# Kernel tuning notes

Hardware: AMD Instinct MI355X
Metric: run time of the kernel (lower is better)

## Reference

```python
import jax, jax.numpy as jnp
import numpy as np
from jax import lax

B, T, H, DEPTH = 32, 2048, 256, 4  # batch, max seq len, hidden, num dilated layers


def setup_inputs() -> dict:
    key = jax.random.key(0)
    k0, k1, k2, k3, k4 = jax.random.split(key, 5)
    x = jax.random.normal(k0, (B, T, H), dtype=jnp.float32)
    # ragged lengths in [T//2, T]
    seq_lens = jax.random.randint(k1, (B,), T // 2, T + 1)
    s = 1.0 / np.sqrt(H)
    Wx = jax.random.uniform(k2, (DEPTH, H, H), jnp.float32, -s, s)
    Wh = jax.random.uniform(k3, (DEPTH, H, H), jnp.float32, -s, s)
    b = jax.random.uniform(k4, (DEPTH, H), jnp.float32, -s, s)
    return {"x": x, "Wx": Wx, "Wh": Wh, "b": b, "seq_lens": seq_lens}


def _dilated_layer(x, Wx, Wh, b, dilation):
    # x: [B, T, H]; recurrence h_k = tanh(x_k @ Wx + h_{k-dilation} @ Wh + b),
    # h_prev = 0 for k < dilation. Positions k mod dilation == r form an
    # independent stream, so reshape into `dilation` interleaved streams and
    # run one scan of length ceil(T/dilation).
    Bn, Tn, Hn = x.shape
    pad = (-Tn) % dilation
    xp = jnp.pad(x, ((0, 0), (0, pad), (0, 0)))
    steps = xp.shape[1] // dilation
    # [steps, B, dilation, H]; element [t, b, r] is timestep t*dilation + r
    xs = jnp.transpose(xp.reshape(Bn, steps, dilation, Hn), (1, 0, 2, 3))
    h0 = jnp.zeros((Bn, dilation, Hn), x.dtype)  # init_state per stream

    def step(h, xt):
        h_new = jnp.tanh(xt @ Wx + h @ Wh + b)
        return h_new, h_new

    _, ys = lax.scan(step, h0, xs)  # [steps, B, dilation, H]
    ys = jnp.transpose(ys, (1, 0, 2, 3)).reshape(Bn, steps * dilation, Hn)
    return ys[:, :Tn]


def reference(x, Wx, Wh, b, seq_lens):
    # Mirrors DilatedRNN.forward: output[i][j][k] for depth j with link_len 2**j.
    # Invalid positions (k >= seq_len) never feed into valid ones (forward-only
    # dilated dependence), so we compute densely and mask at the end.
    depth = Wx.shape[0]
    h = x
    outs = []
    for j in range(depth):
        h = _dilated_layer(h, Wx[j], Wh[j], b[j], 2 ** j)
        outs.append(h)
    out = jnp.stack(outs, axis=1)  # [B, depth, T, H] == output TensorArray
    mask = (jnp.arange(out.shape[2])[None, :] < seq_lens[:, None]).astype(x.dtype)
    return out * mask[:, None, :, None]
```

## Files before the change

kernel.cpp:

```cpp
#include <hip/hip_runtime.h>

#define Bn 32
#define Tn 2048
#define Hn 256
#define DEPTHn 4

typedef _Float16 h2 __attribute__((ext_vector_type(2)));
typedef _Float16 h8 __attribute__((ext_vector_type(8)));

__device__ __forceinline__ h2 pkrtz(float a, float b) {
    return __builtin_bit_cast(h2, __builtin_amdgcn_cvt_pkrtz(a, b));
}

template <int CTRL>
__device__ __forceinline__ float dpp_qp(float x) {
    int xi = __builtin_bit_cast(int, x);
    int r = __builtin_amdgcn_update_dpp(0, xi, CTRL, 0xF, 0xF, true);
    return __builtin_bit_cast(float, r);
}

#define GR 64
__global__ __launch_bounds__(256, 2) void gemm_xw(
    const float* __restrict__ in, long in_bstride,
    const float* __restrict__ Wx, const float* __restrict__ bias,
    float* __restrict__ Z)
{
    __shared__ __align__(16) float a_lds[GR][264];

    const int tid = threadIdx.x;
    const int row0 = blockIdx.x * GR;

    #pragma unroll
    for (int q = 0; q < 16; ++q) {
        int f = tid + q * 256;
        int r  = f >> 6;
        int c4 = f & 63;
        int grow = row0 + r;
        int b = grow >> 11;
        int t = grow & (Tn - 1);
        float4 v = *(const float4*)(in + (long)b * in_bstride + (long)t * Hn + c4 * 4);
        *(float4*)(&a_lds[r][c4 * 4]) = v;
    }
    __syncthreads();

    const int g  = tid >> 5;
    const int cg = tid & 31;

    float acc[8][8];
    #pragma unroll
    for (int i = 0; i < 8; ++i)
        #pragma unroll
        for (int j = 0; j < 8; ++j) acc[i][j] = 0.f;

    for (int k4 = 0; k4 < 64; ++k4) {
        float4 w[4][2];
        #pragma unroll
        for (int kk = 0; kk < 4; ++kk) {
            const float* wr = Wx + (long)(k4 * 4 + kk) * Hn + cg * 8;
            w[kk][0] = *(const float4*)(wr);
            w[kk][1] = *(const float4*)(wr + 4);
        }
        float4 a[8];
        #pragma unroll
        for (int i = 0; i < 8; ++i)
            a[i] = *(const float4*)(&a_lds[i * 8 + g][k4 * 4]);

        #pragma unroll
        for (int i = 0; i < 8; ++i) {
            #pragma unroll
            for (int kk = 0; kk < 4; ++kk) {
                float av = ((const float*)&a[i])[kk];
                acc[i][0] = fmaf(av, w[kk][0].x, acc[i][0]);
                acc[i][1] = fmaf(av, w[kk][0].y, acc[i][1]);
                acc[i][2] = fmaf(av, w[kk][0].z, acc[i][2]);
                acc[i][3] = fmaf(av, w[kk][0].w, acc[i][3]);
                acc[i][4] = fmaf(av, w[kk][1].x, acc[i][4]);
                acc[i][5] = fmaf(av, w[kk][1].y, acc[i][5]);
                acc[i][6] = fmaf(av, w[kk][1].z, acc[i][6]);
                acc[i][7] = fmaf(av, w[kk][1].w, acc[i][7]);
            }
        }
    }

    float4 b0 = *(const float4*)(bias + cg * 8);
    float4 b1 = *(const float4*)(bias + cg * 8 + 4);
    #pragma unroll
    for (int i = 0; i < 8; ++i) {
        long row = row0 + i * 8 + g;
        float4 o0 = { acc[i][0] + b0.x, acc[i][1] + b0.y, acc[i][2] + b0.z, acc[i][3] + b0.w };
        float4 o1 = { acc[i][4] + b1.x, acc[i][5] + b1.y, acc[i][6] + b1.z, acc[i][7] + b1.w };
        *(float4*)(Z + row * Hn + cg * 8)     = o0;
        *(float4*)(Z + row * Hn + cg * 8 + 4) = o1;
    }
}

__global__ __launch_bounds__(512) void rnn_layer(
    const float* __restrict__ Z,
    const float* __restrict__ Wh,
    float* __restrict__ out,
    const int* __restrict__ seq_lens,
    int dilation)
{
    __shared__ __align__(16) h2 hbuf[2 * 144];

    const int tid  = threadIdx.x;
    const int wv   = tid >> 6;
    const int lane = tid & 63;
    const int q    = lane & 3;
    const int c    = lane >> 2;
    const int ch0  = wv * 32 + c;
    const int ch1  = ch0 + 16;

    const int s = blockIdx.x;
    const int b = s / dilation;
    const int r = s % dilation;

    h2 wA[32], wB[32];
    #pragma unroll
    for (int p = 0; p < 32; ++p) {
        int k0 = 64 * q + 2 * p;
        wA[p] = pkrtz(Wh[(long)k0 * Hn + ch0], Wh[(long)(k0 + 1) * Hn + ch0]);
        wB[p] = pkrtz(Wh[(long)k0 * Hn + ch1], Wh[(long)(k0 + 1) * Hn + ch1]);
    }

    if (tid < 288) ((unsigned int*)hbuf)[tid] = 0u;
    const int L = seq_lens[b];
    __syncthreads();

    const float* zb = Z + (long)b * Tn * Hn;
    float* ob = out + (long)b * (DEPTHn * Tn * Hn);

    const int och = (q & 1) ? ch1 : ch0;
    const bool producer = (q < 2);

    int cur = 0;
    float z1 = 0.f, z2 = 0.f;
    if (producer) {
        z1 = zb[(long)r * Hn + och];
        if (r + dilation < Tn) z2 = zb[(long)(r + dilation) * Hn + och];
    }

    for (int t = r; t < Tn; t += dilation) {
        float zc = z1;
        z1 = z2;
        int t2 = t + 2 * dilation;
        if (producer && t2 < Tn) z2 = zb[(long)t2 * Hn + och];

        const h2* hp = &hbuf[cur * 144 + q * 36];
        float a0 = 0.f, a1 = 0.f, a2 = 0.f, a3 = 0.f;
        float b0 = 0.f, b1 = 0.f, b2 = 0.f, b3 = 0.f;
        #pragma unroll
        for (int i4 = 0; i4 < 8; ++i4) {
            h8 hv = *(const h8*)(hp + i4 * 4);
            h2 p0 = __builtin_shufflevector(hv, hv, 0, 1);
            h2 p1 = __builtin_shufflevector(hv, hv, 2, 3);
            h2 p2 = __builtin_shufflevector(hv, hv, 4, 5);
            h2 p3 = __builtin_shufflevector(hv, hv, 6, 7);
            a0 = __builtin_amdgcn_fdot2(p0, wA[i4 * 4 + 0], a0, false);
            a1 = __builtin_amdgcn_fdot2(p1, wA[i4 * 4 + 1], a1, false);
            a2 = __builtin_amdgcn_fdot2(p2, wA[i4 * 4 + 2], a2, false);
            a3 = __builtin_amdgcn_fdot2(p3, wA[i4 * 4 + 3], a3, false);
            b0 = __builtin_amdgcn_fdot2(p0, wB[i4 * 4 + 0], b0, false);
            b1 = __builtin_amdgcn_fdot2(p1, wB[i4 * 4 + 1], b1, false);
            b2 = __builtin_amdgcn_fdot2(p2, wB[i4 * 4 + 2], b2, false);
            b3 = __builtin_amdgcn_fdot2(p3, wB[i4 * 4 + 3], b3, false);
        }
        float pA = (a0 + a1) + (a2 + a3);
        float pB = (b0 + b1) + (b2 + b3);

        pA += dpp_qp<0xB1>(pA);
        pA += dpp_qp<0x4E>(pA);
        pB += dpp_qp<0xB1>(pB);
        pB += dpp_qp<0x4E>(pB);

        if (producer) {
            float ssum = ((q & 1) ? pB : pA) + zc;
            float e = __expf(2.f * ssum);
            float hn = 1.f - 2.f / (e + 1.f);
            ob[(long)t * Hn + och] = (t < L) ? hn : 0.f;
            int m = och >> 1;
            _Float16* hw = (_Float16*)&hbuf[(cur ^ 1) * 144 + (m >> 5) * 36 + (m & 31)];
            hw[och & 1] = (_Float16)hn;
        }

        asm volatile("s_waitcnt lgkmcnt(0)\n\ts_barrier" ::: "memory");
        cur ^= 1;
    }
}

extern "C" void kernel_launch(void* const* d_in, const int* in_sizes, int n_in,
                              void* d_out, int out_size, void* d_ws, size_t ws_size,
                              hipStream_t stream) {
    const float* x    = (const float*)d_in[0];
    const float* Wx   = (const float*)d_in[1];
    const float* Wh   = (const float*)d_in[2];
    const float* bias = (const float*)d_in[3];
    const int*   seq  = (const int*)  d_in[4];
    float* out = (float*)d_out;
    float* Z   = (float*)d_ws;

    for (int j = 0; j < DEPTHn; ++j) {
        const float* in;
        long bstride;
        if (j == 0) { in = x;                             bstride = (long)Tn * Hn; }
        else        { in = out + (long)(j - 1) * Tn * Hn; bstride = (long)DEPTHn * Tn * Hn; }

        hipLaunchKernelGGL(gemm_xw, dim3(Bn * Tn / GR), dim3(256), 0, stream,
                           in, bstride, Wx + (long)j * Hn * Hn, bias + (long)j * Hn, Z);

        int d = 1 << j;
        hipLaunchKernelGGL(rnn_layer, dim3(Bn * d), dim3(512), 0, stream,
                           Z, Wh + (long)j * Hn * Hn, out + (long)j * Tn * Hn, seq, d);
    }
}
```

Measured before the change: 2.615 ms.

## Halve RNN block to 256 threads with four output channels per lane

Shrinks the recurrent kernel from 8 to 4 wavefronts per block. Each lane now holds Wh weights for four channels instead of two (128 packed half2 registers), so all four quad lanes produce an output rather than only two. The goal is cheaper per-step barriers and fewer idle lanes, at the cost of twice the FMA work per lane per step and higher register pressure, which could lengthen the serial critical path.

```diff
diff --git a/kernel.cpp b/kernel.cpp
--- a/kernel.cpp
+++ b/kernel.cpp
@@ -94,7 +94,7 @@
     }
 }
 
-__global__ __launch_bounds__(512) void rnn_layer(
+__global__ __launch_bounds__(256) void rnn_layer(
     const float* __restrict__ Z,
     const float* __restrict__ Wh,
     float* __restrict__ out,
@@ -108,47 +108,48 @@
     const int lane = tid & 63;
     const int q    = lane & 3;
     const int c    = lane >> 2;
-    const int ch0  = wv * 32 + c;
-    const int ch1  = ch0 + 16;
+    const int ch0  = wv * 64 + c;
 
     const int s = blockIdx.x;
     const int b = s / dilation;
     const int r = s % dilation;
 
-    h2 wA[32], wB[32];
+    h2 w0[32], w1[32], w2[32], w3[32];
     #pragma unroll
     for (int p = 0; p < 32; ++p) {
         int k0 = 64 * q + 2 * p;
-        wA[p] = pkrtz(Wh[(long)k0 * Hn + ch0], Wh[(long)(k0 + 1) * Hn + ch0]);
-        wB[p] = pkrtz(Wh[(long)k0 * Hn + ch1], Wh[(long)(k0 + 1) * Hn + ch1]);
-    }
-
-    if (tid < 288) ((unsigned int*)hbuf)[tid] = 0u;
+        const float* wr0 = Wh + (long)k0 * Hn;
+        const float* wr1 = Wh + (long)(k0 + 1) * Hn;
+        w0[p] = pkrtz(wr0[ch0],      wr1[ch0]);
+        w1[p] = pkrtz(wr0[ch0 + 16], wr1[ch0 + 16]);
+        w2[p] = pkrtz(wr0[ch0 + 32], wr1[ch0 + 32]);
+        w3[p] = pkrtz(wr0[ch0 + 48], wr1[ch0 + 48]);
+    }
+
+    ((unsigned int*)hbuf)[tid] = 0u;
+    if (tid < 32) ((unsigned int*)hbuf)[256 + tid] = 0u;
     const int L = seq_lens[b];
     __syncthreads();
 
     const float* zb = Z + (long)b * Tn * Hn;
     float* ob = out + (long)b * (DEPTHn * Tn * Hn);
 
-    const int och = (q & 1) ? ch1 : ch0;
-    const bool producer = (q < 2);
+    const int och = ch0 + 16 * q;
 
     int cur = 0;
-    float z1 = 0.f, z2 = 0.f;
-    if (producer) {
-        z1 = zb[(long)r * Hn + och];
-        if (r + dilation < Tn) z2 = zb[(long)(r + dilation) * Hn + och];
-    }
+    float z1 = zb[(long)r * Hn + och];
+    float z2 = 0.f;
+    if (r + dilation < Tn) z2 = zb[(long)(r + dilation) * Hn + och];
 
     for (int t = r; t < Tn; t += dilation) {
         float zc = z1;
         z1 = z2;
         int t2 = t + 2 * dilation;
-        if (producer && t2 < Tn) z2 = zb[(long)t2 * Hn + och];
+        if (t2 < Tn) z2 = zb[(long)t2 * Hn + och];
 
         const h2* hp = &hbuf[cur * 144 + q * 36];
-        float a0 = 0.f, a1 = 0.f, a2 = 0.f, a3 = 0.f;
-        float b0 = 0.f, b1 = 0.f, b2 = 0.f, b3 = 0.f;
+        float s0a = 0.f, s0b = 0.f, s1a = 0.f, s1b = 0.f;
+        float s2a = 0.f, s2b = 0.f, s3a = 0.f, s3b = 0.f;
         #pragma unroll
         for (int i4 = 0; i4 < 8; ++i4) {
             h8 hv = *(const h8*)(hp + i4 * 4);
@@ -156,32 +157,43 @@
             h2 p1 = __builtin_shufflevector(hv, hv, 2, 3);
             h2 p2 = __builtin_shufflevector(hv, hv, 4, 5);
             h2 p3 = __builtin_shufflevector(hv, hv, 6, 7);
-            a0 = __builtin_amdgcn_fdot2(p0, wA[i4 * 4 + 0], a0, false);
-            a1 = __builtin_amdgcn_fdot2(p1, wA[i4 * 4 + 1], a1, false);
-            a2 = __builtin_amdgcn_fdot2(p2, wA[i4 * 4 + 2], a2, false);
-            a3 = __builtin_amdgcn_fdot2(p3, wA[i4 * 4 + 3], a3, false);
-            b0 = __builtin_amdgcn_fdot2(p0, wB[i4 * 4 + 0], b0, false);
-            b1 = __builtin_amdgcn_fdot2(p1, wB[i4 * 4 + 1], b1, false);
-            b2 = __builtin_amdgcn_fdot2(p2, wB[i4 * 4 + 2], b2, false);
-            b3 = __builtin_amdgcn_fdot2(p3, wB[i4 * 4 + 3], b3, false);
+            s0a = __builtin_amdgcn_fdot2(p0, w0[i4 * 4 + 0], s0a, false);
+            s0b = __builtin_amdgcn_fdot2(p1, w0[i4 * 4 + 1], s0b, false);
+            s0a = __builtin_amdgcn_fdot2(p2, w0[i4 * 4 + 2], s0a, false);
+            s0b = __builtin_amdgcn_fdot2(p3, w0[i4 * 4 + 3], s0b, false);
+            s1a = __builtin_amdgcn_fdot2(p0, w1[i4 * 4 + 0], s1a, false);
+            s1b = __builtin_amdgcn_fdot2(p1, w1[i4 * 4 + 1], s1b, false);
+            s1a = __builtin_amdgcn_fdot2(p2, w1[i4 * 4 + 2], s1a, false);
+            s1b = __builtin_amdgcn_fdot2(p3, w1[i4 * 4 + 3], s1b, false);
+            s2a = __builtin_amdgcn_fdot2(p0, w2[i4 * 4 + 0], s2a, false);
+            s2b = __builtin_amdgcn_fdot2(p1, w2[i4 * 4 + 1], s2b, false);
+            s2a = __builtin_amdgcn_fdot2(p2, w2[i4 * 4 + 2], s2a, false);
+            s2b = __builtin_amdgcn_fdot2(p3, w2[i4 * 4 + 3], s2b, false);
+            s3a = __builtin_amdgcn_fdot2(p0, w3[i4 * 4 + 0], s3a, false);
+            s3b = __builtin_amdgcn_fdot2(p1, w3[i4 * 4 + 1], s3b, false);
+            s3a = __builtin_amdgcn_fdot2(p2, w3[i4 * 4 + 2], s3a, false);
+            s3b = __builtin_amdgcn_fdot2(p3, w3[i4 * 4 + 3], s3b, false);
         }
-        float pA = (a0 + a1) + (a2 + a3);
-        float pB = (b0 + b1) + (b2 + b3);
-
-        pA += dpp_qp<0xB1>(pA);
-        pA += dpp_qp<0x4E>(pA);
-        pB += dpp_qp<0xB1>(pB);
-        pB += dpp_qp<0x4E>(pB);
-
-        if (producer) {
-            float ssum = ((q & 1) ? pB : pA) + zc;
-            float e = __expf(2.f * ssum);
-            float hn = 1.f - 2.f / (e + 1.f);
-            ob[(long)t * Hn + och] = (t < L) ? hn : 0.f;
-            int m = och >> 1;
-            _Float16* hw = (_Float16*)&hbuf[(cur ^ 1) * 144 + (m >> 5) * 36 + (m & 31)];
-            hw[och & 1] = (_Float16)hn;
-        }
+        float s0 = s0a + s0b;
+        float s1 = s1a + s1b;
+        float s2 = s2a + s2b;
+        float s3 = s3a + s3b;
+
+        s0 += dpp_qp<0xB1>(s0);  s0 += dpp_qp<0x4E>(s0);
+        s1 += dpp_qp<0xB1>(s1);  s1 += dpp_qp<0x4E>(s1);
+        s2 += dpp_qp<0xB1>(s2);  s2 += dpp_qp<0x4E>(s2);
+        s3 += dpp_qp<0xB1>(s3);  s3 += dpp_qp<0x4E>(s3);
+
+        float se = (q & 2) ? ((q & 1) ? s3 : s2) : ((q & 1) ? s1 : s0);
+
+        float ssum = se + zc;
+        float e = __expf(2.f * ssum);
+        float hn = 1.f - 2.f / (e + 1.f);
+        ob[(long)t * Hn + och] = (t < L) ? hn : 0.f;
+
+        int m = och >> 1;
+        _Float16* hw = (_Float16*)&hbuf[(cur ^ 1) * 144 + (m >> 5) * 36 + (m & 31)];
+        hw[och & 1] = (_Float16)hn;
 
         asm volatile("s_waitcnt lgkmcnt(0)\n\ts_barrier" ::: "memory");
         cur ^= 1;
@@ -209,7 +221,7 @@
                            in, bstride, Wx + (long)j * Hn * Hn, bias + (long)j * Hn, Z);
 
         int d = 1 << j;
-        hipLaunchKernelGGL(rnn_layer, dim3(Bn * d), dim3(512), 0, stream,
+        hipLaunchKernelGGL(rnn_layer, dim3(Bn * d), dim3(256), 0, stream,
                            Z, Wh + (long)j * Hn * Hn, out + (long)j * Tn * Hn, seq, d);
     }
 }
```

New measurement: 2.497 ms. 1.05x faster.
